# Kernel optimization log

Measured on AMD Instinct MI355X. Metric: run time of the kernel, lower is better.

## Reference

```python
import jax, jax.numpy as jnp
import numpy as np
from functools import partial
from jax import lax

K = 3
CIN = 64
COUT = 128
D = 4
H_STEP = 1.0
EPS = 1e-8
SCALE = 1.0


@partial(jax.custom_vjp, nondiff_argnums=(1,))
def spike_fn(x, scale):
    # SurrogateHeaviside forward: hard step
    return (x > 0).astype(x.dtype)


def _spike_fwd(x, scale):
    return spike_fn(x, scale), x


def _spike_bwd(scale, x, g):
    # surrogate gradient: derivative of sigmoid(scale * x)
    sig = jax.nn.sigmoid(scale * x)
    return (g * scale * sig * (1.0 - sig),)


spike_fn.defvjp(_spike_fwd, _spike_bwd)


def setup_inputs() -> dict:
    key = jax.random.key(0)
    k1, k2, k3, k4 = jax.random.split(key, 4)
    x = jax.random.normal(k1, (32, CIN, 64, 64), dtype=jnp.float32)
    mem = jnp.zeros((32, COUT, 64, 64), dtype=jnp.float32)
    # ME kernel layout: [K*K, Cin, Cout]; xavier-ish scale
    kernel = jax.random.normal(k2, (K * K, CIN, COUT), dtype=jnp.float32) * 0.05
    beta = 0.8 + 0.01 * jax.random.normal(k3, (1,), dtype=jnp.float32)
    b = 0.1 + 0.01 * jax.random.normal(k4, (COUT,), dtype=jnp.float32)
    return {"x": x, "mem": mem, "kernel": kernel, "beta": beta, "b": b, "bs": 32}


def reference(x, mem, kernel, beta, b, bs):
    # sparse conv densified -> plain strided conv on dense input
    w = kernel.reshape(K, K, CIN, COUT).transpose(3, 2, 0, 1)  # OIHW
    conv_dense = lax.conv_general_dilated(
        x, w, window_strides=(1, 1), padding="SAME",
        dimension_numbers=("NCHW", "OIHW", "NCHW"))  # [bs, Cout, H, W]

    # LIF membrane update
    new_mem = mem * beta + conv_dense * (1.0 - beta)

    # per-out-channel kernel norm scaling, minus threshold bias
    norm = jnp.sum(kernel ** 2, axis=(0, 1))  # [Cout]
    mthr = new_mem / (norm + EPS)[None, :, None, None] - b[None, :, None, None]

    # multi-threshold spike count
    spk = jnp.zeros_like(mthr)
    for d in range(D):
        spk = spk + spike_fn(mthr - d * H_STEP, SCALE)

    spk_mask = (spk > 0).astype(new_mem.dtype)
    final_mem = new_mem * (1.0 - spk_mask)
    return spk, final_mem
```

## Files before the change

### kernel.cpp

```cpp
#include <hip/hip_runtime.h>


typedef _Float16 half8 __attribute__((ext_vector_type(8)));
typedef float f32x4 __attribute__((ext_vector_type(4)));

constexpr int CIc = 64, COc = 128, HHc = 64, WWc = 64, NBc = 32;
constexpr float EPSB = 2e-4f;
constexpr unsigned CAPc = 1u << 18;

constexpr size_t O_CNT   = 0;
constexpr size_t O_NORMD = 16;
constexpr size_t O_RNORM = O_NORMD + 1024;
constexpr size_t O_WDT   = O_RNORM + 512;
constexpr size_t O_WHI   = O_WDT + 589824;
constexpr size_t O_WLO   = O_WHI + 147456;
constexpr size_t O_LIST  = O_WLO + 147456;
constexpr size_t WS_NEED = O_LIST + (size_t)CAPc * 4;

__global__ void prep_kernel(const float* __restrict__ w, double* __restrict__ normd,
                            float* __restrict__ rnormf, double* __restrict__ wdT,
                            _Float16* __restrict__ whi, _Float16* __restrict__ wlo,
                            unsigned* __restrict__ counter) {
    const int bx = blockIdx.x;
    if (bx < 128) {
        const int co = bx, lane = threadIdx.x & 63;
        if (threadIdx.x >= 64) return;
        double s = 0.0;
        #pragma unroll
        for (int k = 0; k < 9; ++k) {
            const double v = (double)w[(k * 64 + lane) * COc + co];
            s = fma(v, v, s);
        }
        #pragma unroll
        for (int off = 32; off; off >>= 1) s += __shfl_xor(s, off);
        if (lane == 0) {
            s += 1e-8;
            normd[co]  = s;
            rnormf[co] = (float)(1.0 / s);
            if (co == 0) counter[0] = 0u;
        }
    } else {
        const int i = (bx - 128) * 256 + threadIdx.x;
        if (i >= 9 * CIc * COc) return;
        const int ci = i & 63, t = (i >> 6) % 9, co = i / (9 * 64);
        const float v = w[(t * CIc + ci) * COc + co];
        wdT[i] = (double)v;
        if (whi) {
            const int i2 = (t * COc + co) * CIc + ci;
            const _Float16 h = (_Float16)v;
            whi[i2] = h;
            wlo[i2] = (_Float16)(v - (float)h);
        }
    }
}

__global__ __launch_bounds__(256, 2) void convM(
    const float* __restrict__ x,
    const float* __restrict__ mem,
    const _Float16* __restrict__ whi,
    const _Float16* __restrict__ wlo,
    const float* __restrict__ beta_p,
    const float* __restrict__ bias,
    const float* __restrict__ rnormf,
    float* __restrict__ out_spk, float* __restrict__ out_mem,
    unsigned* __restrict__ counter, unsigned* __restrict__ list)
{
    __shared__ half8 xs[4224];
    char* xsb = (char*)(&xs[0]);

    const int tid = threadIdx.x;
    const int y0 = blockIdx.x * 8;
    const int cohalf = blockIdx.y;
    const int n = blockIdx.z;

    const int lane   = tid & 63;
    const int wv     = tid >> 6;
    const int co0    = cohalf * 64 + wv * 16;
    const int lanelo = lane & 15;
    const int kgi    = (lane >> 4) * 8;
    const unsigned kg2 = (unsigned)(lane >> 4) * 16;

    half8 wH[9][2], wL[9][2];
    {
        const int co = co0 + lanelo;
        const _Float16* wh = whi + (size_t)co * CIc + kgi;
        const _Float16* wl = wlo + (size_t)co * CIc + kgi;
        #pragma unroll
        for (int t = 0; t < 9; ++t)
            #pragma unroll
            for (int cs = 0; cs < 2; ++cs) {
                wH[t][cs] = *(const half8*)(wh + (size_t)t * COc * CIc + cs * 32);
                wL[t][cs] = *(const half8*)(wl + (size_t)t * COc * CIc + cs * 32);
            }
    }

    auto stage = [&](int rabs) {
        const int slot = (rabs + 8) & 3;
        char* sb = xsb + slot * 16896;
        float v[3][8];
        #pragma unroll
        for (int c = 0; c < 3; ++c) {
            const int it = tid + c * 256;
            if (it < 528) {
                const int px1 = it % 66, cig = it / 66;
                const int px = px1 - 1;
                const bool val = ((unsigned)px < 64u) && ((unsigned)rabs < 64u);
                const float* xp = x + (((size_t)n * CIc + cig * 8) * HHc
                                       + (val ? rabs : 0)) * WWc + (val ? px : 0);
                #pragma unroll
                for (int j = 0; j < 8; ++j)
                    v[c][j] = val ? xp[j * (HHc * WWc)] : 0.0f;
            }
        }
        #pragma unroll
        for (int c = 0; c < 3; ++c) {
            const int it = tid + c * 256;
            if (it < 528) {
                const int px1 = it % 66, cig = it / 66;
                half8 hv, lv;
                #pragma unroll
                for (int j = 0; j < 8; ++j) {
                    const float f = v[c][j];
                    const _Float16 h = (_Float16)f;
                    hv[j] = h;
                    lv[j] = (_Float16)(f - (float)h);
                }
                const unsigned off = (unsigned)px1 * 128
                                   + (((unsigned)cig * 16) ^ (((unsigned)px1 & 7) << 4));
                *(half8*)(sb + off)        = hv;
                *(half8*)(sb + 8448 + off) = lv;
            }
        }
    };

    stage(y0 - 1);
    stage(y0);
    stage(y0 + 1);
    __syncthreads();

    const float beta = beta_p[0];
    const float omb  = 1.0f - beta;
    float rnv[4], biv[4];
    #pragma unroll
    for (int r = 0; r < 4; ++r) {
        const int co = co0 + (lane >> 4) * 4 + r;
        rnv[r] = rnormf[co];
        biv[r] = bias[co];
    }

    for (int j = 0; j < 8; ++j) {
        const int y = y0 + j;

        if (j < 7) stage(y + 2);

        float mv[4][4];
        #pragma unroll
        for (int r = 0; r < 4; ++r) {
            const int co = co0 + (lane >> 4) * 4 + r;
            const float* mp = mem + (((size_t)n * COc + co) * HHc + y) * WWc + lanelo;
            #pragma unroll
            for (int pf = 0; pf < 4; ++pf) mv[r][pf] = mp[pf * 16];
        }

        f32x4 acc[4];
        #pragma unroll
        for (int pf = 0; pf < 4; ++pf) acc[pf] = f32x4{0.f, 0.f, 0.f, 0.f};

        #pragma unroll
        for (int t = 0; t < 9; ++t) {
            const int dy = t / 3, dx = t % 3;
            const unsigned sbase = (unsigned)((y - 1 + dy + 8) & 3) * 16896;
            #pragma unroll
            for (int cs = 0; cs < 2; ++cs) {
                #pragma unroll
                for (int pf = 0; pf < 4; ++pf) {
                    const int px1 = pf * 16 + lanelo + dx;
                    const unsigned ob = sbase + (unsigned)px1 * 128
                        + (((unsigned)(cs * 64) + kg2) ^ (((unsigned)px1 & 7) << 4));
                    const half8 bh = *(const half8*)(xsb + ob);
                    const half8 bl = *(const half8*)(xsb + 8448 + ob);
                    acc[pf] = __builtin_amdgcn_mfma_f32_16x16x32_f16(wH[t][cs], bh, acc[pf], 0, 0, 0);
                    acc[pf] = __builtin_amdgcn_mfma_f32_16x16x32_f16(wH[t][cs], bl, acc[pf], 0, 0, 0);
                    acc[pf] = __builtin_amdgcn_mfma_f32_16x16x32_f16(wL[t][cs], bh, acc[pf], 0, 0, 0);
                }
            }
        }

        #pragma unroll
        for (int pf = 0; pf < 4; ++pf) {
            const int px = pf * 16 + lanelo;
            #pragma unroll
            for (int r = 0; r < 4; ++r) {
                const int co = co0 + (lane >> 4) * 4 + r;
                const size_t idx = (((size_t)n * COc + co) * HHc + y) * WWc + px;
                const float nm   = fmaf(mv[r][pf], beta, acc[pf][r] * omb);
                const float mthr = fmaf(nm, rnv[r], -biv[r]);
                const int s = (mthr > 0.f) + (mthr > 1.f) + (mthr > 2.f) + (mthr > 3.f);
                out_spk[idx] = (float)s;
                out_mem[idx] = (s > 0) ? 0.0f : nm;

                const bool fl = (fabsf(mthr) < EPSB) | (fabsf(mthr - 1.f) < EPSB) |
                                (fabsf(mthr - 2.f) < EPSB) | (fabsf(mthr - 3.f) < EPSB);
                const unsigned long long msk = __ballot(fl);
                if (msk) {
                    unsigned wb = 0;
                    if (lane == 0) wb = atomicAdd(counter, (unsigned)__popcll(msk));
                    wb = __shfl(wb, 0);
                    if (fl) {
                        const unsigned pos =
                            wb + (unsigned)__popcll(msk & ((1ull << lane) - 1ull));
                        if (pos < CAPc) list[pos] = (unsigned)idx;
                    }
                }
            }
        }

        __syncthreads();
    }
}

__global__ __launch_bounds__(256) void fixB(
    const float* __restrict__ x, const float* __restrict__ mem,
    const float* __restrict__ beta_p, const float* __restrict__ bias,
    const double* __restrict__ normd, const double* __restrict__ wdT,
    const unsigned* __restrict__ counter, const unsigned* __restrict__ list,
    float* __restrict__ out_spk, float* __restrict__ out_mem)
{
    const int lane  = threadIdx.x & 63;
    const int wave  = blockIdx.x * 4 + (threadIdx.x >> 6);
    const int nwave = gridDim.x * 4;
    const unsigned cnt = min(counter[0], CAPc);
    const double beta = (double)beta_p[0];
    const double omb  = 1.0 - beta;

    for (unsigned p = wave; p < cnt; p += nwave) {
        const unsigned idx = list[p];
        const int xp = idx & 63, yp = (idx >> 6) & 63;
        const int co = (idx >> 12) & 127, n = idx >> 19;

        const float*  xc = x + ((size_t)n * CIc + lane) * (HHc * WWc);
        const double* wt = wdT + (size_t)co * 9 * CIc + lane;

        double a = 0.0;
        #pragma unroll
        for (int t = 0; t < 9; ++t) {
            const int yy = yp + t / 3 - 1, xx = xp + t % 3 - 1;
            const bool v = ((unsigned)yy < 64u) && ((unsigned)xx < 64u);
            const int yyc = min(max(yy, 0), 63), xxc = min(max(xx, 0), 63);
            const double xv = v ? (double)xc[yyc * WWc + xxc] : 0.0;
            a = fma(xv, wt[t * CIc], a);
        }
        #pragma unroll
        for (int off = 32; off; off >>= 1) a += __shfl_xor(a, off);

        if (lane == 0) {
            const double nm   = (double)mem[idx] * beta + a * omb;
            const double mthr = nm / normd[co] - (double)bias[co];
            const int s = (mthr > 0.) + (mthr > 1.) + (mthr > 2.) + (mthr > 3.);
            out_spk[idx] = (float)s;
            out_mem[idx] = (s > 0) ? 0.0f : (float)nm;
        }
    }
}

__global__ __launch_bounds__(256) void conv_fp64_fb(
    const float* __restrict__ x, const float* __restrict__ mem,
    const float* __restrict__ w, const float* __restrict__ beta_p,
    const float* __restrict__ bias, const double* __restrict__ normd,
    float* __restrict__ out_spk, float* __restrict__ out_mem)
{
    const int ix = threadIdx.x, iy = blockIdx.x * 4 + threadIdx.y;
    const int co0 = blockIdx.y * 8, n = blockIdx.z;
    bool valid[9]; int xoff[9];
    #pragma unroll
    for (int kh = 0; kh < 3; ++kh) {
        const int yy = iy + kh - 1;
        #pragma unroll
        for (int kw = 0; kw < 3; ++kw) {
            const int xx = ix + kw - 1, t = kh * 3 + kw;
            valid[t] = ((unsigned)yy < 64u) && ((unsigned)xx < 64u);
            xoff[t]  = yy * WWc + xx;
        }
    }
    double acc[8];
    #pragma unroll
    for (int j = 0; j < 8; ++j) acc[j] = 0.0;
    const float* xb = x + (size_t)n * CIc * HHc * WWc;
    for (int ci = 0; ci < CIc; ++ci) {
        const float* xc = xb + (size_t)ci * HHc * WWc;
        #pragma unroll
        for (int t = 0; t < 9; ++t) {
            const double xv = valid[t] ? (double)xc[xoff[t]] : 0.0;
            const float* wt = w + ((size_t)t * CIc + ci) * COc + co0;
            #pragma unroll
            for (int j = 0; j < 8; ++j) acc[j] = fma(xv, (double)wt[j], acc[j]);
        }
    }
    const double beta = (double)beta_p[0], omb = 1.0 - beta;
    const size_t base = (((size_t)n * COc + co0) * HHc + iy) * WWc + ix;
    #pragma unroll
    for (int j = 0; j < 8; ++j) {
        const size_t idx = base + (size_t)j * (HHc * WWc);
        const double nm   = (double)mem[idx] * beta + acc[j] * omb;
        const double mthr = nm / normd[co0 + j] - (double)bias[co0 + j];
        const int s = (mthr > 0.) + (mthr > 1.) + (mthr > 2.) + (mthr > 3.);
        out_spk[idx] = (float)s;
        out_mem[idx] = (s > 0) ? 0.0f : (float)nm;
    }
}

extern "C" void kernel_launch(void* const* d_in, const int* in_sizes, int n_in,
                              void* d_out, int out_size, void* d_ws, size_t ws_size,
                              hipStream_t stream) {
    const float* x      = (const float*)d_in[0];
    const float* mem    = (const float*)d_in[1];
    const float* w      = (const float*)d_in[2];
    const float* beta_p = (const float*)d_in[3];
    const float* bias   = (const float*)d_in[4];

    float* out_spk = (float*)d_out;
    float* out_mem = out_spk + (size_t)NBc * COc * HHc * WWc;

    char* ws = (char*)d_ws;
    unsigned* counter = (unsigned*)(ws + O_CNT);
    double*   normd   = (double*)(ws + O_NORMD);
    float*    rnormf  = (float*)(ws + O_RNORM);
    double*   wdT     = (double*)(ws + O_WDT);
    _Float16* whi     = (_Float16*)(ws + O_WHI);
    _Float16* wlo     = (_Float16*)(ws + O_WLO);
    unsigned* list    = (unsigned*)(ws + O_LIST);

    if (ws_size >= WS_NEED) {
        prep_kernel<<<128 + 288, 256, 0, stream>>>(w, normd, rnormf, wdT, whi, wlo,
                                                   counter);
        dim3 grdM(8, 2, NBc);
        convM<<<grdM, 256, 0, stream>>>(x, mem, whi, wlo, beta_p, bias, rnormf,
                                        out_spk, out_mem, counter, list);
        fixB<<<512, 256, 0, stream>>>(x, mem, beta_p, bias, normd, wdT,
                                      counter, list, out_spk, out_mem);
    } else {
        prep_kernel<<<128, 256, 0, stream>>>(w, normd, rnormf, wdT, nullptr, nullptr,
                                             counter);
        dim3 blk(WWc, 4, 1);
        dim3 grd(HHc / 4, COc / 8, NBc);
        conv_fp64_fb<<<grd, blk, 0, stream>>>(x, mem, w, beta_p, bias, normd,
                                              out_spk, out_mem);
    }
}
```

Before: 412.9 us.

## Software-pipeline input row loads and batch ballots in the spike epilogue

```diff
diff --git a/kernel.cpp b/kernel.cpp
--- a/kernel.cpp
+++ b/kernel.cpp
@@ -5,7 +5,7 @@
 typedef float f32x4 __attribute__((ext_vector_type(4)));
 
 constexpr int CIc = 64, COc = 128, HHc = 64, WWc = 64, NBc = 32;
-constexpr float EPSB = 2e-4f;
+constexpr float EPSB = 5e-5f;
 constexpr unsigned CAPc = 1u << 18;
 
 constexpr size_t O_CNT   = 0;
@@ -94,10 +94,9 @@
             }
     }
 
-    auto stage = [&](int rabs) {
-        const int slot = (rabs + 8) & 3;
-        char* sb = xsb + slot * 16896;
-        float v[3][8];
+    float xr[3][8];
+
+    auto issueRow = [&](int rabs) {
         #pragma unroll
         for (int c = 0; c < 3; ++c) {
             const int it = tid + c * 256;
@@ -108,10 +107,14 @@
                 const float* xp = x + (((size_t)n * CIc + cig * 8) * HHc
                                        + (val ? rabs : 0)) * WWc + (val ? px : 0);
                 #pragma unroll
-                for (int j = 0; j < 8; ++j)
-                    v[c][j] = val ? xp[j * (HHc * WWc)] : 0.0f;
-            }
-        }
+                for (int j2 = 0; j2 < 8; ++j2)
+                    xr[c][j2] = val ? xp[j2 * (HHc * WWc)] : 0.0f;
+            }
+        }
+    };
+    auto writeRow = [&](int rabs) {
+        const int slot = (rabs + 8) & 3;
+        char* sb = xsb + slot * 16896;
         #pragma unroll
         for (int c = 0; c < 3; ++c) {
             const int it = tid + c * 256;
@@ -119,11 +122,11 @@
                 const int px1 = it % 66, cig = it / 66;
                 half8 hv, lv;
                 #pragma unroll
-                for (int j = 0; j < 8; ++j) {
-                    const float f = v[c][j];
+                for (int j2 = 0; j2 < 8; ++j2) {
+                    const float f = xr[c][j2];
                     const _Float16 h = (_Float16)f;
-                    hv[j] = h;
-                    lv[j] = (_Float16)(f - (float)h);
+                    hv[j2] = h;
+                    lv[j2] = (_Float16)(f - (float)h);
                 }
                 const unsigned off = (unsigned)px1 * 128
                                    + (((unsigned)cig * 16) ^ (((unsigned)px1 & 7) << 4));
@@ -133,10 +136,12 @@
         }
     };
 
-    stage(y0 - 1);
-    stage(y0);
-    stage(y0 + 1);
-    __syncthreads();
+    issueRow(y0 - 1); writeRow(y0 - 1);
+    issueRow(y0);     writeRow(y0);
+    issueRow(y0 + 1); writeRow(y0 + 1);
+    issueRow(y0 + 2);
+    asm volatile("s_waitcnt lgkmcnt(0)" ::: "memory");
+    __builtin_amdgcn_s_barrier();
 
     const float beta = beta_p[0];
     const float omb  = 1.0f - beta;
@@ -151,7 +156,8 @@
     for (int j = 0; j < 8; ++j) {
         const int y = y0 + j;
 
-        if (j < 7) stage(y + 2);
+        if (j < 7) writeRow(y + 2);
+        if (j < 6) issueRow(y + 3);
 
         float mv[4][4];
         #pragma unroll
@@ -166,6 +172,7 @@
         #pragma unroll
         for (int pf = 0; pf < 4; ++pf) acc[pf] = f32x4{0.f, 0.f, 0.f, 0.f};
 
+        __builtin_amdgcn_s_setprio(1);
         #pragma unroll
         for (int t = 0; t < 9; ++t) {
             const int dy = t / 3, dx = t % 3;
@@ -185,7 +192,9 @@
                 }
             }
         }
-
+        __builtin_amdgcn_s_setprio(0);
+
+        unsigned flm = 0u;
         #pragma unroll
         for (int pf = 0; pf < 4; ++pf) {
             const int px = pf * 16 + lanelo;
@@ -195,27 +204,43 @@
                 const size_t idx = (((size_t)n * COc + co) * HHc + y) * WWc + px;
                 const float nm   = fmaf(mv[r][pf], beta, acc[pf][r] * omb);
                 const float mthr = fmaf(nm, rnv[r], -biv[r]);
-                const int s = (mthr > 0.f) + (mthr > 1.f) + (mthr > 2.f) + (mthr > 3.f);
-                out_spk[idx] = (float)s;
-                out_mem[idx] = (s > 0) ? 0.0f : nm;
-
-                const bool fl = (fabsf(mthr) < EPSB) | (fabsf(mthr - 1.f) < EPSB) |
-                                (fabsf(mthr - 2.f) < EPSB) | (fabsf(mthr - 3.f) < EPSB);
-                const unsigned long long msk = __ballot(fl);
-                if (msk) {
-                    unsigned wb = 0;
-                    if (lane == 0) wb = atomicAdd(counter, (unsigned)__popcll(msk));
-                    wb = __shfl(wb, 0);
-                    if (fl) {
-                        const unsigned pos =
-                            wb + (unsigned)__popcll(msk & ((1ull << lane) - 1ull));
-                        if (pos < CAPc) list[pos] = (unsigned)idx;
+                const float cm = fminf(fmaxf(ceilf(mthr), 0.0f), 4.0f);
+                out_spk[idx] = cm;
+                out_mem[idx] = (cm > 0.0f) ? 0.0f : nm;
+                const float fr = rintf(mthr);
+                const bool fl = (fabsf(mthr - fr) < EPSB) &
+                                (fr >= 0.0f) & (fr <= 3.5f);
+                flm |= ((unsigned)fl) << (pf * 4 + r);
+            }
+        }
+        if (__ballot(flm != 0u)) {
+            #pragma unroll
+            for (int pf = 0; pf < 4; ++pf) {
+                #pragma unroll
+                for (int r = 0; r < 4; ++r) {
+                    const unsigned long long msk =
+                        __ballot((flm >> (pf * 4 + r)) & 1u);
+                    if (msk) {
+                        unsigned wb = 0;
+                        if (lane == 0)
+                            wb = atomicAdd(counter, (unsigned)__popcll(msk));
+                        wb = __shfl(wb, 0);
+                        if ((flm >> (pf * 4 + r)) & 1u) {
+                            const int px = pf * 16 + lanelo;
+                            const int co = co0 + (lane >> 4) * 4 + r;
+                            const size_t idx =
+                                (((size_t)n * COc + co) * HHc + y) * WWc + px;
+                            const unsigned pos = wb +
+                                (unsigned)__popcll(msk & ((1ull << lane) - 1ull));
+                            if (pos < CAPc) list[pos] = (unsigned)idx;
+                        }
                     }
                 }
             }
         }
 
-        __syncthreads();
+        asm volatile("s_waitcnt lgkmcnt(0)" ::: "memory");
+        __builtin_amdgcn_s_barrier();
     }
 }
 
```

Result: faster. 354.4 us (-14.2%).
